# Performance work log

Hardware: AMD Instinct MI355X
Metric: run time of the kernel (lower is better)

Reference implementation:

```python
import jax, jax.numpy as jnp
import numpy as np

H = 64  # hidden size


def _lstm_layer(x_seq, h0, c0, Wih, Whh, bih, bhh):
    """x_seq: (B,S,I); returns (out (B,S,H), h_final (B,H), c_final (B,H)).
    Gate order matches torch nn.LSTM: i, f, g, o."""
    # Precompute input projections for all timesteps (one big GEMM).
    xproj = jnp.einsum('bsi,gi->bsg', x_seq, Wih) + bih + bhh  # (B,S,4H)

    def step(carry, xp):
        h, c = carry
        gates = xp + h @ Whh.T  # (B,4H)
        i = jax.nn.sigmoid(gates[:, 0 * H:1 * H])
        f = jax.nn.sigmoid(gates[:, 1 * H:2 * H])
        g = jnp.tanh(gates[:, 2 * H:3 * H])
        o = jax.nn.sigmoid(gates[:, 3 * H:4 * H])
        c = f * c + i * g
        h = o * jnp.tanh(c)
        return (h, c), h

    (hT, cT), hs = jax.lax.scan(step, (h0, c0), xproj.transpose(1, 0, 2))
    return hs.transpose(1, 0, 2), hT, cT


def setup_inputs() -> dict:
    key = jax.random.key(0)
    ks = jax.random.split(key, 12)
    B, S, I = 256, 2048, 32
    s_in = 1.0 / np.sqrt(H)
    inp = {
        'x': jax.random.normal(ks[0], (B, S, I), dtype=jnp.float32),
        'h0': jnp.zeros((2, B, H), dtype=jnp.float32),
        'c0': jnp.zeros((2, B, H), dtype=jnp.float32),
        # layer 0 params (torch layout: W_ih (4H,I), W_hh (4H,H))
        'Wih0': jax.random.uniform(ks[1], (4 * H, I), jnp.float32, -s_in, s_in),
        'Whh0': jax.random.uniform(ks[2], (4 * H, H), jnp.float32, -s_in, s_in),
        'bih0': jax.random.uniform(ks[3], (4 * H,), jnp.float32, -s_in, s_in),
        'bhh0': jax.random.uniform(ks[4], (4 * H,), jnp.float32, -s_in, s_in),
        # layer 1 params (input is H)
        'Wih1': jax.random.uniform(ks[5], (4 * H, H), jnp.float32, -s_in, s_in),
        'Whh1': jax.random.uniform(ks[6], (4 * H, H), jnp.float32, -s_in, s_in),
        'bih1': jax.random.uniform(ks[7], (4 * H,), jnp.float32, -s_in, s_in),
        'bhh1': jax.random.uniform(ks[8], (4 * H,), jnp.float32, -s_in, s_in),
        # head
        'Wh': jax.random.uniform(ks[9], (1, H), jnp.float32, -s_in, s_in),
        'bh': jax.random.uniform(ks[10], (1,), jnp.float32, -s_in, s_in),
    }
    return inp


def reference(x, h0, c0, Wih0, Whh0, bih0, bhh0, Wih1, Whh1, bih1, bhh1, Wh, bh):
    # Layer 0
    out0, h_f0, c_f0 = _lstm_layer(x, h0[0], c0[0], Wih0, Whh0, bih0, bhh0)
    # Inter-layer dropout is inactive in eval mode -> identity.
    # Layer 1
    out1, h_f1, c_f1 = _lstm_layer(out0, h0[1], c0[1], Wih1, Whh1, bih1, bhh1)
    probs = jax.nn.sigmoid(out1 @ Wh.T + bh)  # (B,S,1)
    h = jnp.stack([h_f0, h_f1], axis=0)  # (2,B,H)
    c = jnp.stack([c_f0, c_f1], axis=0)
    return probs, h, c
```

## Files before the change

### kernel.cpp

```cpp
#include <hip/hip_runtime.h>
#include <math.h>
#include <stdint.h>

#define SS 2048
#define II 32
#define TB 4

typedef _Float16 f16x8  __attribute__((ext_vector_type(8)));
typedef float    f32x4  __attribute__((ext_vector_type(4)));
typedef uint32_t u32x4e __attribute__((ext_vector_type(4)));
typedef _Float16 f16x2  __attribute__((ext_vector_type(2)));
typedef __fp16   g16x2  __attribute__((ext_vector_type(2)));

union uhc { uint32_t u; f16x2 a; g16x2 b; };
union frag { f16x8 v; uint32_t w[4]; u32x4e q; };

__device__ __forceinline__ uint32_t pk(float x, float y) {
    uhc c; c.b = __builtin_amdgcn_cvt_pkrtz(x, y); return c.u;
}
__device__ __forceinline__ float fdot2(uint32_t a, uint32_t b, float c) {
    uhc x, y; x.u = a; y.u = b;
#if __has_builtin(__builtin_amdgcn_fdot2)
    return __builtin_amdgcn_fdot2(x.a, y.a, c, false);
#else
    return c + (float)x.a.x * (float)y.a.x + (float)x.a.y * (float)y.a.y;
#endif
}
__device__ __forceinline__ float sigm(float x) { return __builtin_amdgcn_rcpf(1.f + __expf(-x)); }
__device__ __forceinline__ float tanh_(float x) {
    x = fminf(fmaxf(x, -15.f), 15.f);
    float e = __expf(-2.f * x);
    return (1.f - e) * __builtin_amdgcn_rcpf(1.f + e);
}
__device__ __forceinline__ frag load8(const float* p) {
    float4 v0 = ((const float4*)p)[0];
    float4 v1 = ((const float4*)p)[1];
    frag f;
    f.w[0] = pk(v0.x, v0.y); f.w[1] = pk(v0.z, v0.w);
    f.w[2] = pk(v1.x, v1.y); f.w[3] = pk(v1.z, v1.w);
    return f;
}
#define MFMA(A, B, C) __builtin_amdgcn_mfma_f32_16x16x32_f16((A).v, (B).v, (C), 0, 0, 0)
#define EXTR(A) (jhi ? (jlo ? (A)[3] : (A)[2]) : (jlo ? (A)[1] : (A)[0]))

#define STAGE(c) do {                                                               \
    if (tid < 256) {                                                                \
        const int t0_ = (c) * 16;                                                   \
        const int s_ = tid >> 4, g_ = (tid >> 2) & 3, bb_ = tid & 3;                \
        const float* p_ = x + (size_t)(bbase + bb_) * (SS * II)                     \
                          + (size_t)(t0_ + s_) * II + g_ * 8;                       \
        float4 v0_ = ((const float4*)p_)[0];                                        \
        float4 v1_ = ((const float4*)p_)[1];                                        \
        u32x4e wv_ = { pk(v0_.x, v0_.y), pk(v0_.z, v0_.w),                          \
                       pk(v1_.x, v1_.y), pk(v1_.z, v1_.w) };                        \
        *(u32x4e*)((char*)&xsb[(c) & 1][s_][0] + (g_ * 4 + bb_) * 16) = wv_;        \
    } } while (0)

__global__ __launch_bounds__(512, 1) void lstm_mfma(
    const float* __restrict__ x,
    const float* __restrict__ h_in, const float* __restrict__ c_in,
    const float* __restrict__ Wih0, const float* __restrict__ Whh0,
    const float* __restrict__ bih0, const float* __restrict__ bhh0,
    const float* __restrict__ Wih1, const float* __restrict__ Whh1,
    const float* __restrict__ bih1, const float* __restrict__ bhh1,
    const float* __restrict__ Wh, const float* __restrict__ bh,
    float* __restrict__ out)
{
    __shared__ uint32_t hbuf[2][2][128];
    __shared__ uint32_t xsb[2][16][64];
    __shared__ float    pbuf[64][4];

    const int tid = threadIdx.x;
    const int w   = tid >> 6, L = tid & 63;
    const int wl  = w & 3;
    const int g16 = L >> 4, b16 = L & 15;
    const int bb  = b16 & 3, j = b16 >> 2;
    const int isL1 = (w >= 4);
    const int u    = 16 * wl + g16 * 4 + j;
    const int bbase = blockIdx.x * TB;
    const int loff  = isL1 ? 16384 : 0;
    const bool jlo = (j & 1) != 0, jhi = (j & 2) != 0;
    const int hoff = ((u >> 3) * 4 + bb) * 16 + (u & 7) * 2;

    float hst = h_in[loff + (size_t)(bbase + bb) * 64 + u];
    float cst = c_in[loff + (size_t)(bbase + bb) * 64 + u];
    {
        float o = __shfl_xor(hst, 4);
        if (!jlo) *(uint32_t*)((char*)&hbuf[1][isL1][0] + hoff) = pk(hst, o);
    }
    STAGE(0);
    __syncthreads();

    if (!isL1) {
        frag aH[4][2], aX[4];
        f32x4 bias4[4];
        #pragma unroll
        for (int t = 0; t < 4; ++t) {
            const int arow = t * 64 + 16 * wl + b16;
            aH[t][0] = load8(Whh0 + arow * 64 + g16 * 8);
            aH[t][1] = load8(Whh0 + arow * 64 + 32 + g16 * 8);
            aX[t]    = load8(Wih0 + arow * 32 + g16 * 8);
            const int brow = t * 64 + 16 * wl + g16 * 4;
            float4 q1 = *(const float4*)(bih0 + brow);
            float4 q2 = *(const float4*)(bhh0 + brow);
            bias4[t] = (f32x4){q1.x + q2.x, q1.y + q2.y, q1.z + q2.z, q1.w + q2.w};
        }

        #pragma unroll 1
        for (int it = 0; it <= SS + 1; ++it) {
            if (it < SS) {
                const char* hb = (const char*)&hbuf[(it + 1) & 1][0][0];
                frag bh0, bh1, bx;
                bh0.v = *(const f16x8*)(hb + (g16 * 4 + bb) * 16);
                bh1.v = *(const f16x8*)(hb + ((4 + g16) * 4 + bb) * 16);
                bx.v  = *(const f16x8*)((const char*)&xsb[(it >> 4) & 1][it & 15][0]
                                        + (g16 * 4 + bb) * 16);
                f32x4 a0 = bias4[0], a1 = bias4[1], a2 = bias4[2], a3 = bias4[3];
                a0 = MFMA(aH[0][0], bh0, a0); a1 = MFMA(aH[1][0], bh0, a1);
                a2 = MFMA(aH[2][0], bh0, a2); a3 = MFMA(aH[3][0], bh0, a3);
                a0 = MFMA(aH[0][1], bh1, a0); a1 = MFMA(aH[1][1], bh1, a1);
                a2 = MFMA(aH[2][1], bh1, a2); a3 = MFMA(aH[3][1], bh1, a3);
                a0 = MFMA(aX[0], bx, a0);     a1 = MFMA(aX[1], bx, a1);
                a2 = MFMA(aX[2], bx, a2);     a3 = MFMA(aX[3], bx, a3);
                float gi = sigm(EXTR(a0)), gf = sigm(EXTR(a1));
                float gg = tanh_(EXTR(a2)), go = sigm(EXTR(a3));
                cst = gf * cst + gi * gg;
                hst = go * tanh_(cst);
                float o = __shfl_xor(hst, 4);
                if (!jlo) *(uint32_t*)((char*)&hbuf[it & 1][0][0] + hoff) = pk(hst, o);
            }
            if ((it & 15) == 0 && it + 16 < SS) STAGE((it >> 4) + 1);
            __syncthreads();
        }
    } else {
        frag aI[4][2], aR[4][2];
        f32x4 bias4[4];
        #pragma unroll
        for (int t = 0; t < 4; ++t) {
            const int arow = t * 64 + 16 * wl + b16;
            aI[t][0] = load8(Wih1 + arow * 64 + g16 * 8);
            aI[t][1] = load8(Wih1 + arow * 64 + 32 + g16 * 8);
            aR[t][0] = load8(Whh1 + arow * 64 + g16 * 8);
            aR[t][1] = load8(Whh1 + arow * 64 + 32 + g16 * 8);
            const int brow = t * 64 + 16 * wl + g16 * 4;
            float4 q1 = *(const float4*)(bih1 + brow);
            float4 q2 = *(const float4*)(bhh1 + brow);
            bias4[t] = (f32x4){q1.x + q2.x, q1.y + q2.y, q1.z + q2.z, q1.w + q2.w};
        }
        frag whA = load8(Wh + g16 * 8);
        frag whB = load8(Wh + 32 + g16 * 8);
        const float bhs = bh[0];

        #pragma unroll 1
        for (int it = 0; it <= SS + 1; ++it) {
            frag b1, b1k;
            if (it >= 1) {
                const char* h1b = (const char*)&hbuf[it & 1][1][0];
                b1.v  = *(const f16x8*)(h1b + (g16 * 4 + bb) * 16);
                b1k.v = *(const f16x8*)(h1b + ((4 + g16) * 4 + bb) * 16);
            }
            if (it >= 1 && it <= SS) {
                const char* h0b = (const char*)&hbuf[(it + 1) & 1][0][0];
                frag b0, b0k;
                b0.v  = *(const f16x8*)(h0b + (g16 * 4 + bb) * 16);
                b0k.v = *(const f16x8*)(h0b + ((4 + g16) * 4 + bb) * 16);
                f32x4 a0 = bias4[0], a1 = bias4[1], a2 = bias4[2], a3 = bias4[3];
                a0 = MFMA(aI[0][0], b0, a0);  a1 = MFMA(aI[1][0], b0, a1);
                a2 = MFMA(aI[2][0], b0, a2);  a3 = MFMA(aI[3][0], b0, a3);
                a0 = MFMA(aI[0][1], b0k, a0); a1 = MFMA(aI[1][1], b0k, a1);
                a2 = MFMA(aI[2][1], b0k, a2); a3 = MFMA(aI[3][1], b0k, a3);
                a0 = MFMA(aR[0][0], b1, a0);  a1 = MFMA(aR[1][0], b1, a1);
                a2 = MFMA(aR[2][0], b1, a2);  a3 = MFMA(aR[3][0], b1, a3);
                a0 = MFMA(aR[0][1], b1k, a0); a1 = MFMA(aR[1][1], b1k, a1);
                a2 = MFMA(aR[2][1], b1k, a2); a3 = MFMA(aR[3][1], b1k, a3);
                float gi = sigm(EXTR(a0)), gf = sigm(EXTR(a1));
                float gg = tanh_(EXTR(a2)), go = sigm(EXTR(a3));
                cst = gf * cst + gi * gg;
                hst = go * tanh_(cst);
                float o = __shfl_xor(hst, 4);
                if (!jlo) *(uint32_t*)((char*)&hbuf[(it + 1) & 1][1][0] + hoff) = pk(hst, o);
            }
            if (w == 4 && it >= 2) {
                float pv = 0.f;
                #pragma unroll
                for (int i = 0; i < 4; ++i) {
                    pv = fdot2(whA.w[i], b1.w[i], pv);
                    pv = fdot2(whB.w[i], b1k.w[i], pv);
                }
                pv += __shfl_xor(pv, 16);
                pv += __shfl_xor(pv, 32);
                pv = sigm(pv + bhs);
                const int t = it - 2;
                if (L < 4) pbuf[t & 63][L] = pv;
                if ((t & 63) == 63) {
                    const int tbase = t & ~63;
                    const int fb = L >> 4, fs = (L & 15) * 4;
                    float4 vv = make_float4(pbuf[fs][fb], pbuf[fs + 1][fb],
                                            pbuf[fs + 2][fb], pbuf[fs + 3][fb]);
                    *(float4*)(out + (size_t)(bbase + fb) * SS + tbase + fs) = vv;
                }
            }
            __syncthreads();
        }
    }

    out[524288 + loff + (size_t)(bbase + bb) * 64 + u] = hst;
    out[557056 + loff + (size_t)(bbase + bb) * 64 + u] = cst;
}

extern "C" void kernel_launch(void* const* d_in, const int* in_sizes, int n_in,
                              void* d_out, int out_size, void* d_ws, size_t ws_size,
                              hipStream_t stream) {
    const float* x    = (const float*)d_in[0];
    const float* h0   = (const float*)d_in[1];
    const float* c0   = (const float*)d_in[2];
    const float* Wih0 = (const float*)d_in[3];
    const float* Whh0 = (const float*)d_in[4];
    const float* bih0 = (const float*)d_in[5];
    const float* bhh0 = (const float*)d_in[6];
    const float* Wih1 = (const float*)d_in[7];
    const float* Whh1 = (const float*)d_in[8];
    const float* bih1 = (const float*)d_in[9];
    const float* bhh1 = (const float*)d_in[10];
    const float* Wh   = (const float*)d_in[11];
    const float* bh   = (const float*)d_in[12];
    float* out = (float*)d_out;

    hipLaunchKernelGGL(lstm_mfma, dim3(256 / TB), dim3(512), 0, stream,
                       x, h0, c0, Wih0, Whh0, bih0, bhh0,
                       Wih1, Whh1, bih1, bhh1, Wh, bh, out);
}
```

Baseline: 1.389 ms.

## Split MFMA chains, prefetch x into registers, move head to layer-0 wave

The per-step MFMA accumulation is split into two independent chains that are summed afterwards, which shortens the dependent MFMA latency on the recurrent critical path. The h writeback now stores one fp16 per lane instead of a shuffle plus packed store. The global load of x is issued early into registers and written to LDS half a chunk later, so load latency is hidden. The output-head dot product is moved from a layer-1 wave to wave 0, which takes it off the slower layer-1 path. Loops are unrolled by 2. The risks are extra register pressure and sub-dword LDS stores.

```diff
diff --git a/kernel.cpp b/kernel.cpp
--- a/kernel.cpp
+++ b/kernel.cpp
@@ -42,19 +42,6 @@
 }
 #define MFMA(A, B, C) __builtin_amdgcn_mfma_f32_16x16x32_f16((A).v, (B).v, (C), 0, 0, 0)
 #define EXTR(A) (jhi ? (jlo ? (A)[3] : (A)[2]) : (jlo ? (A)[1] : (A)[0]))
-
-#define STAGE(c) do {                                                               \
-    if (tid < 256) {                                                                \
-        const int t0_ = (c) * 16;                                                   \
-        const int s_ = tid >> 4, g_ = (tid >> 2) & 3, bb_ = tid & 3;                \
-        const float* p_ = x + (size_t)(bbase + bb_) * (SS * II)                     \
-                          + (size_t)(t0_ + s_) * II + g_ * 8;                       \
-        float4 v0_ = ((const float4*)p_)[0];                                        \
-        float4 v1_ = ((const float4*)p_)[1];                                        \
-        u32x4e wv_ = { pk(v0_.x, v0_.y), pk(v0_.z, v0_.w),                          \
-                       pk(v1_.x, v1_.y), pk(v1_.z, v1_.w) };                        \
-        *(u32x4e*)((char*)&xsb[(c) & 1][s_][0] + (g_ * 4 + bb_) * 16) = wv_;        \
-    } } while (0)
 
 __global__ __launch_bounds__(512, 1) void lstm_mfma(
     const float* __restrict__ x,
@@ -82,13 +69,20 @@
     const bool jlo = (j & 1) != 0, jhi = (j & 2) != 0;
     const int hoff = ((u >> 3) * 4 + bb) * 16 + (u & 7) * 2;
 
+    const f32x4 zf4 = {0.f, 0.f, 0.f, 0.f};
+
     float hst = h_in[loff + (size_t)(bbase + bb) * 64 + u];
     float cst = c_in[loff + (size_t)(bbase + bb) * 64 + u];
-    {
-        float o = __shfl_xor(hst, 4);
-        if (!jlo) *(uint32_t*)((char*)&hbuf[1][isL1][0] + hoff) = pk(hst, o);
+    *(__fp16*)((char*)&hbuf[1][isL1][0] + hoff) = (__fp16)hst;
+
+    if (tid < 256) {
+        const int s_ = tid >> 4, g_ = (tid >> 2) & 3, bb_ = tid & 3;
+        const float* p_ = x + (size_t)(bbase + bb_) * (SS * II) + (size_t)s_ * II + g_ * 8;
+        float4 v0_ = ((const float4*)p_)[0];
+        float4 v1_ = ((const float4*)p_)[1];
+        u32x4e wv_ = { pk(v0_.x, v0_.y), pk(v0_.z, v0_.w), pk(v1_.x, v1_.y), pk(v1_.z, v1_.w) };
+        *(u32x4e*)((char*)&xsb[0][s_][0] + (g_ * 4 + bb_) * 16) = wv_;
     }
-    STAGE(0);
     __syncthreads();
 
     if (!isL1) {
@@ -105,9 +99,21 @@
             float4 q2 = *(const float4*)(bhh0 + brow);
             bias4[t] = (f32x4){q1.x + q2.x, q1.y + q2.y, q1.z + q2.z, q1.w + q2.w};
         }
-
-        #pragma unroll 1
+        frag whA = load8(Wh + g16 * 8);
+        frag whB = load8(Wh + 32 + g16 * 8);
+        const float bhs = bh[0];
+
+        float4 xr0, xr1;
+        const int s_ = tid >> 4, g_ = (tid >> 2) & 3, bb_ = tid & 3;
+        const float* xsrc_base = x + (size_t)(bbase + bb_) * (SS * II) + (size_t)s_ * II + g_ * 8;
+
+        #pragma unroll 2
         for (int it = 0; it <= SS + 1; ++it) {
+            if ((it & 15) == 0 && it + 16 < SS) {
+                const float* p_ = xsrc_base + (size_t)(((it >> 4) + 1) * 16) * II;
+                xr0 = ((const float4*)p_)[0];
+                xr1 = ((const float4*)p_)[1];
+            }
             if (it < SS) {
                 const char* hb = (const char*)&hbuf[(it + 1) & 1][0][0];
                 frag bh0, bh1, bx;
@@ -115,72 +121,25 @@
                 bh1.v = *(const f16x8*)(hb + ((4 + g16) * 4 + bb) * 16);
                 bx.v  = *(const f16x8*)((const char*)&xsb[(it >> 4) & 1][it & 15][0]
                                         + (g16 * 4 + bb) * 16);
-                f32x4 a0 = bias4[0], a1 = bias4[1], a2 = bias4[2], a3 = bias4[3];
-                a0 = MFMA(aH[0][0], bh0, a0); a1 = MFMA(aH[1][0], bh0, a1);
-                a2 = MFMA(aH[2][0], bh0, a2); a3 = MFMA(aH[3][0], bh0, a3);
-                a0 = MFMA(aH[0][1], bh1, a0); a1 = MFMA(aH[1][1], bh1, a1);
-                a2 = MFMA(aH[2][1], bh1, a2); a3 = MFMA(aH[3][1], bh1, a3);
-                a0 = MFMA(aX[0], bx, a0);     a1 = MFMA(aX[1], bx, a1);
-                a2 = MFMA(aX[2], bx, a2);     a3 = MFMA(aX[3], bx, a3);
+                f32x4 p0 = bias4[0], p1 = bias4[1], p2 = bias4[2], p3 = bias4[3];
+                p0 = MFMA(aH[0][0], bh0, p0); p1 = MFMA(aH[1][0], bh0, p1);
+                p2 = MFMA(aH[2][0], bh0, p2); p3 = MFMA(aH[3][0], bh0, p3);
+                p0 = MFMA(aX[0], bx, p0);     p1 = MFMA(aX[1], bx, p1);
+                p2 = MFMA(aX[2], bx, p2);     p3 = MFMA(aX[3], bx, p3);
+                f32x4 q0 = MFMA(aH[0][1], bh1, zf4), q1 = MFMA(aH[1][1], bh1, zf4);
+                f32x4 q2 = MFMA(aH[2][1], bh1, zf4), q3 = MFMA(aH[3][1], bh1, zf4);
+                f32x4 a0 = p0 + q0, a1 = p1 + q1, a2 = p2 + q2, a3 = p3 + q3;
                 float gi = sigm(EXTR(a0)), gf = sigm(EXTR(a1));
                 float gg = tanh_(EXTR(a2)), go = sigm(EXTR(a3));
                 cst = gf * cst + gi * gg;
                 hst = go * tanh_(cst);
-                float o = __shfl_xor(hst, 4);
-                if (!jlo) *(uint32_t*)((char*)&hbuf[it & 1][0][0] + hoff) = pk(hst, o);
-            }
-            if ((it & 15) == 0 && it + 16 < SS) STAGE((it >> 4) + 1);
-            __syncthreads();
-        }
-    } else {
-        frag aI[4][2], aR[4][2];
-        f32x4 bias4[4];
-        #pragma unroll
-        for (int t = 0; t < 4; ++t) {
-            const int arow = t * 64 + 16 * wl + b16;
-            aI[t][0] = load8(Wih1 + arow * 64 + g16 * 8);
-            aI[t][1] = load8(Wih1 + arow * 64 + 32 + g16 * 8);
-            aR[t][0] = load8(Whh1 + arow * 64 + g16 * 8);
-            aR[t][1] = load8(Whh1 + arow * 64 + 32 + g16 * 8);
-            const int brow = t * 64 + 16 * wl + g16 * 4;
-            float4 q1 = *(const float4*)(bih1 + brow);
-            float4 q2 = *(const float4*)(bhh1 + brow);
-            bias4[t] = (f32x4){q1.x + q2.x, q1.y + q2.y, q1.z + q2.z, q1.w + q2.w};
-        }
-        frag whA = load8(Wh + g16 * 8);
-        frag whB = load8(Wh + 32 + g16 * 8);
-        const float bhs = bh[0];
-
-        #pragma unroll 1
-        for (int it = 0; it <= SS + 1; ++it) {
-            frag b1, b1k;
-            if (it >= 1) {
+                *(__fp16*)((char*)&hbuf[it & 1][0][0] + hoff) = (__fp16)hst;
+            }
+            if (w == 0 && it >= 2) {
                 const char* h1b = (const char*)&hbuf[it & 1][1][0];
+                frag b1, b1k;
                 b1.v  = *(const f16x8*)(h1b + (g16 * 4 + bb) * 16);
                 b1k.v = *(const f16x8*)(h1b + ((4 + g16) * 4 + bb) * 16);
-            }
-            if (it >= 1 && it <= SS) {
-                const char* h0b = (const char*)&hbuf[(it + 1) & 1][0][0];
-                frag b0, b0k;
-                b0.v  = *(const f16x8*)(h0b + (g16 * 4 + bb) * 16);
-                b0k.v = *(const f16x8*)(h0b + ((4 + g16) * 4 + bb) * 16);
-                f32x4 a0 = bias4[0], a1 = bias4[1], a2 = bias4[2], a3 = bias4[3];
-                a0 = MFMA(aI[0][0], b0, a0);  a1 = MFMA(aI[1][0], b0, a1);
-                a2 = MFMA(aI[2][0], b0, a2);  a3 = MFMA(aI[3][0], b0, a3);
-                a0 = MFMA(aI[0][1], b0k, a0); a1 = MFMA(aI[1][1], b0k, a1);
-                a2 = MFMA(aI[2][1], b0k, a2); a3 = MFMA(aI[3][1], b0k, a3);
-                a0 = MFMA(aR[0][0], b1, a0);  a1 = MFMA(aR[1][0], b1, a1);
-                a2 = MFMA(aR[2][0], b1, a2);  a3 = MFMA(aR[3][0], b1, a3);
-                a0 = MFMA(aR[0][1], b1k, a0); a1 = MFMA(aR[1][1], b1k, a1);
-                a2 = MFMA(aR[2][1], b1k, a2); a3 = MFMA(aR[3][1], b1k, a3);
-                float gi = sigm(EXTR(a0)), gf = sigm(EXTR(a1));
-                float gg = tanh_(EXTR(a2)), go = sigm(EXTR(a3));
-                cst = gf * cst + gi * gg;
-                hst = go * tanh_(cst);
-                float o = __shfl_xor(hst, 4);
-                if (!jlo) *(uint32_t*)((char*)&hbuf[(it + 1) & 1][1][0] + hoff) = pk(hst, o);
-            }
-            if (w == 4 && it >= 2) {
                 float pv = 0.f;
                 #pragma unroll
                 for (int i = 0; i < 4; ++i) {
@@ -200,6 +159,56 @@
                     *(float4*)(out + (size_t)(bbase + fb) * SS + tbase + fs) = vv;
                 }
             }
+            if ((it & 15) == 8 && it + 8 < SS) {
+                const int cn = (it >> 4) + 1;
+                u32x4e wv_ = { pk(xr0.x, xr0.y), pk(xr0.z, xr0.w),
+                               pk(xr1.x, xr1.y), pk(xr1.z, xr1.w) };
+                *(u32x4e*)((char*)&xsb[cn & 1][s_][0] + (g_ * 4 + bb_) * 16) = wv_;
+            }
+            __syncthreads();
+        }
+    } else {
+        frag aI[4][2], aR[4][2];
+        f32x4 bias4[4];
+        #pragma unroll
+        for (int t = 0; t < 4; ++t) {
+            const int arow = t * 64 + 16 * wl + b16;
+            aI[t][0] = load8(Wih1 + arow * 64 + g16 * 8);
+            aI[t][1] = load8(Wih1 + arow * 64 + 32 + g16 * 8);
+            aR[t][0] = load8(Whh1 + arow * 64 + g16 * 8);
+            aR[t][1] = load8(Whh1 + arow * 64 + 32 + g16 * 8);
+            const int brow = t * 64 + 16 * wl + g16 * 4;
+            float4 q1 = *(const float4*)(bih1 + brow);
+            float4 q2 = *(const float4*)(bhh1 + brow);
+            bias4[t] = (f32x4){q1.x + q2.x, q1.y + q2.y, q1.z + q2.z, q1.w + q2.w};
+        }
+
+        #pragma unroll 2
+        for (int it = 0; it <= SS + 1; ++it) {
+            if (it >= 1 && it <= SS) {
+                const char* h1b = (const char*)&hbuf[it & 1][1][0];
+                const char* h0b = (const char*)&hbuf[(it + 1) & 1][0][0];
+                frag b0, b0k, b1, b1k;
+                b0.v  = *(const f16x8*)(h0b + (g16 * 4 + bb) * 16);
+                b0k.v = *(const f16x8*)(h0b + ((4 + g16) * 4 + bb) * 16);
+                b1.v  = *(const f16x8*)(h1b + (g16 * 4 + bb) * 16);
+                b1k.v = *(const f16x8*)(h1b + ((4 + g16) * 4 + bb) * 16);
+                f32x4 p0 = bias4[0], p1 = bias4[1], p2 = bias4[2], p3 = bias4[3];
+                p0 = MFMA(aI[0][0], b0, p0);  p1 = MFMA(aI[1][0], b0, p1);
+                p2 = MFMA(aI[2][0], b0, p2);  p3 = MFMA(aI[3][0], b0, p3);
+                p0 = MFMA(aR[0][0], b1, p0);  p1 = MFMA(aR[1][0], b1, p1);
+                p2 = MFMA(aR[2][0], b1, p2);  p3 = MFMA(aR[3][0], b1, p3);
+                f32x4 q0 = MFMA(aI[0][1], b0k, zf4), q1 = MFMA(aI[1][1], b0k, zf4);
+                f32x4 q2 = MFMA(aI[2][1], b0k, zf4), q3 = MFMA(aI[3][1], b0k, zf4);
+                q0 = MFMA(aR[0][1], b1k, q0); q1 = MFMA(aR[1][1], b1k, q1);
+                q2 = MFMA(aR[2][1], b1k, q2); q3 = MFMA(aR[3][1], b1k, q3);
+                f32x4 a0 = p0 + q0, a1 = p1 + q1, a2 = p2 + q2, a3 = p3 + q3;
+                float gi = sigm(EXTR(a0)), gf = sigm(EXTR(a1));
+                float gg = tanh_(EXTR(a2)), go = sigm(EXTR(a3));
+                cst = gf * cst + gi * gg;
+                hst = go * tanh_(cst);
+                *(__fp16*)((char*)&hbuf[(it + 1) & 1][1][0] + hoff) = (__fp16)hst;
+            }
             __syncthreads();
         }
     }
```

New measurement: 1.203 ms. 1.15x faster.
